# Performance work log

Measured on AMD Instinct MI355X. Metric: run time of the kernel, lower is better.

The kernel has to match this reference:

```python
import jax, jax.numpy as jnp
import numpy as np

S, B, D_DEC, D_ALIGN, D_ENC = 1024, 64, 1024, 1024, 1024


def setup_inputs() -> dict:
    key = jax.random.key(0)
    ks = jax.random.split(key, 6)
    scale = 1.0 / np.sqrt(D_DEC)
    return {
        "s_tm1": jax.random.normal(ks[0], (B, D_DEC), jnp.float32),
        "xs_h": jax.random.normal(ks[1], (S, B, D_ENC), jnp.float32),
        "uh": jax.random.normal(ks[2], (S, B, D_ALIGN), jnp.float32),
        "xs_mask": jnp.ones((S, B), jnp.float32),
        "sa_w": jax.random.normal(ks[3], (D_ALIGN, D_DEC), jnp.float32) * scale,
        "sa_b": jnp.zeros((D_ALIGN,), jnp.float32),
        "a1_w": jax.random.normal(ks[4], (1, D_ALIGN), jnp.float32) * scale,
        "a1_b": jnp.zeros((1,), jnp.float32),
    }


def reference(s_tm1, xs_h, uh, xs_mask, sa_w, sa_b, a1_w, a1_b):
    # sa(s_tm1): [B, align]
    sa_s = s_tm1 @ sa_w.T + sa_b
    # broadcast-add over seq dim, tanh, then a1 (align -> 1), squeeze -> [S, B]
    h = jnp.tanh(sa_s[None, :, :] + uh)                  # [S, B, align]
    e = jnp.einsum('sba,a->sb', h, a1_w[0]) + a1_b[0]    # [S, B]
    # masked softmax over dim 0 (seq)
    ex = jnp.exp(e - jnp.max(e, axis=0, keepdims=True))
    ex = ex * xs_mask
    e_ij = ex / jnp.sum(ex, axis=0, keepdims=True)       # [S, B]
    # weighted sum over seq: [B, D_enc]
    attend = jnp.einsum('sb,sbd->bd', e_ij, xs_h)
    return (e_ij, attend)
```

## Files before the change

### kernel.cpp

```cpp
#include <hip/hip_runtime.h>
#include <hip/hip_bf16.h>

#define S_DIM 1024
#define B_DIM 64
#define A_DIM 1024

#define K2_CONST 2.8853900817779268f

#define K_TILE 64
#define KSPLIT 16
#define A_TILE 64
#define SSPLIT 8
#define S_CHUNK 128
#define NIT (S_CHUNK / 4)

typedef float f4 __attribute__((ext_vector_type(4)));

__device__ __forceinline__ float fast_exp2(float x) { return __builtin_amdgcn_exp2f(x); }
__device__ __forceinline__ float fast_rcp(float x)  { return __builtin_amdgcn_rcpf(x); }

__global__ __launch_bounds__(256) void gemm_partial_kernel(
    const float* __restrict__ s_tm1,
    const float* __restrict__ sa_w,
    float* __restrict__ part)
{
    __shared__ float sW[K_TILE][68];
    __shared__ float sS[K_TILE][68];
    const int a0 = blockIdx.x * A_TILE;
    const int k0 = blockIdx.y * K_TILE;
    const int t  = threadIdx.x;

    #pragma unroll
    for (int i = 0; i < 4; ++i) {
        int idx = t + 256 * i;
        int row = idx >> 4;
        int c4  = (idx & 15) * 4;
        f4 v = __builtin_nontemporal_load((const f4*)(sa_w + (size_t)(a0 + row) * 1024 + k0 + c4));
        sW[c4 + 0][row] = v.x; sW[c4 + 1][row] = v.y;
        sW[c4 + 2][row] = v.z; sW[c4 + 3][row] = v.w;
        f4 u = *(const f4*)(s_tm1 + (size_t)row * 1024 + k0 + c4);
        sS[c4 + 0][row] = u.x; sS[c4 + 1][row] = u.y;
        sS[c4 + 2][row] = u.z; sS[c4 + 3][row] = u.w;
    }
    __syncthreads();

    const int ta = (t & 15) * 4;
    const int tb = (t >> 4) * 4;
    float acc[4][4] = {};
    #pragma unroll 8
    for (int k = 0; k < K_TILE; ++k) {
        f4 wa = *(const f4*)&sW[k][ta];
        f4 sb = *(const f4*)&sS[k][tb];
        float wv[4] = {wa.x, wa.y, wa.z, wa.w};
        float sv[4] = {sb.x, sb.y, sb.z, sb.w};
        #pragma unroll
        for (int i = 0; i < 4; ++i)
            #pragma unroll
            for (int j = 0; j < 4; ++j)
                acc[i][j] = fmaf(wv[i], sv[j], acc[i][j]);
    }

    float* outp = part + (size_t)blockIdx.y * (B_DIM * 1024);
    #pragma unroll
    for (int j = 0; j < 4; ++j) {
        f4 v = {acc[0][j], acc[1][j], acc[2][j], acc[3][j]};
        *(f4*)(outp + (size_t)(tb + j) * 1024 + a0 + ta) = v;
    }
}

__global__ __launch_bounds__(256) void gemm_reduce_kernel(
    const float* __restrict__ part, const float* __restrict__ sa_b,
    float* __restrict__ ksa)
{
    int idx = blockIdx.x * 256 + threadIdx.x;
    int a = idx & 1023;
    float s = sa_b[a];
    #pragma unroll
    for (int kz = 0; kz < KSPLIT; ++kz)
        s += part[(size_t)kz * 65536 + idx];
    ksa[idx] = K2_CONST * s;
}

template <int AUX>
__device__ __forceinline__ void stage_row(const float* g, float* lds_base, int lane) {
    #pragma unroll
    for (int j = 0; j < 4; ++j) {
        __builtin_amdgcn_global_load_lds(
            (const void*)(g + lane * 4 + j * 256),
            (void*)((char*)lds_base + j * 1024),
            16, 0, AUX);
    }
}

__global__ __launch_bounds__(256) void fused_kernel(
    const float* __restrict__ uh,
    const float* __restrict__ xs_h,
    const float* __restrict__ ksa,
    const float* __restrict__ a1_w,
    const float* __restrict__ xs_mask,
    float* __restrict__ ex_buf,
    float* __restrict__ psum,
    float* __restrict__ part)
{
    const int b    = blockIdx.x;
    const int sz   = blockIdx.y;
    const int s0   = sz * S_CHUNK;
    const int t    = threadIdx.x;
    const int lane = t & 63;
    const int w    = t >> 6;

    __shared__ float s_stage[4][4][1024];
    __shared__ float s_ex[S_CHUNK];
    __shared__ float s_mask[S_CHUNK];

    if (t < S_CHUNK) s_mask[t] = xs_mask[(size_t)(s0 + t) * B_DIM + b];

    const f4* sap = (const f4*)(ksa + (size_t)b * 1024);
    const f4* awp = (const f4*)a1_w;
    f4 sv[4], aw[4];
    #pragma unroll
    for (int j = 0; j < 4; ++j) { sv[j] = sap[lane + 64 * j]; aw[j] = awp[lane + 64 * j]; }

    __syncthreads();

    f4 acc4[4];
    #pragma unroll
    for (int j = 0; j < 4; ++j) { acc4[j].x = 0.f; acc4[j].y = 0.f; acc4[j].z = 0.f; acc4[j].w = 0.f; }

    {
        const size_t ro = ((size_t)(s0 + w) * B_DIM + b) * 1024;
        stage_row<2>(uh + ro,   &s_stage[w][0][0], lane);
        stage_row<0>(xs_h + ro, &s_stage[w][2][0], lane);
    }

    #pragma unroll 1
    for (int k = 0; k < NIT; ++k) {
        const int cur = k & 1;
        const int nxt = cur ^ 1;
        const int i   = w + 4 * k;

        const int kn = (k < NIT - 1) ? (k + 1) : (NIT - 1);
        const size_t rn = ((size_t)(s0 + w + 4 * kn) * B_DIM + b) * 1024;
        stage_row<2>(uh + rn,   &s_stage[w][nxt][0], lane);
        stage_row<0>(xs_h + rn, &s_stage[w][2 + nxt][0], lane);

        asm volatile("s_waitcnt vmcnt(8)" ::: "memory");
        __builtin_amdgcn_sched_barrier(0);

        const f4* ub = (const f4*)&s_stage[w][cur][0];
        const f4* xb = (const f4*)&s_stage[w][2 + cur][0];
        f4 u[4], x[4];
        #pragma unroll
        for (int j = 0; j < 4; ++j) { u[j] = ub[lane + 64 * j]; x[j] = xb[lane + 64 * j]; }

        float acc = 0.f;
        #pragma unroll
        for (int j = 0; j < 4; ++j) {
            float t0 = fast_exp2(fmaf(K2_CONST, u[j].x, sv[j].x));
            float t1 = fast_exp2(fmaf(K2_CONST, u[j].y, sv[j].y));
            float t2 = fast_exp2(fmaf(K2_CONST, u[j].z, sv[j].z));
            float t3 = fast_exp2(fmaf(K2_CONST, u[j].w, sv[j].w));
            acc = fmaf(aw[j].x, fast_rcp(1.0f + t0), acc);
            acc = fmaf(aw[j].y, fast_rcp(1.0f + t1), acc);
            acc = fmaf(aw[j].z, fast_rcp(1.0f + t2), acc);
            acc = fmaf(aw[j].w, fast_rcp(1.0f + t3), acc);
        }
        #pragma unroll
        for (int off = 32; off; off >>= 1) acc += __shfl_xor(acc, off);

        float ex = fast_exp2(-K2_CONST * acc) * s_mask[i];
        if (lane == 0) s_ex[i] = ex;

        #pragma unroll
        for (int j = 0; j < 4; ++j) {
            acc4[j].x = fmaf(ex, x[j].x, acc4[j].x);
            acc4[j].y = fmaf(ex, x[j].y, acc4[j].y);
            acc4[j].z = fmaf(ex, x[j].z, acc4[j].z);
            acc4[j].w = fmaf(ex, x[j].w, acc4[j].w);
        }
    }

    asm volatile("s_waitcnt vmcnt(0)" ::: "memory");
    __builtin_amdgcn_sched_barrier(0);

    f4* red = (f4*)&s_stage[w][0][0];
    #pragma unroll
    for (int j = 0; j < 4; ++j) red[lane + 64 * j] = acc4[j];
    __syncthreads();

    f4 r = ((const f4*)&s_stage[0][0][0])[t];
    #pragma unroll
    for (int ww = 1; ww < 4; ++ww) {
        f4 q = ((const f4*)&s_stage[ww][0][0])[t];
        r.x += q.x; r.y += q.y; r.z += q.z; r.w += q.w;
    }
    ((f4*)part)[((size_t)sz * B_DIM + b) * 256 + t] = r;

    if (t < S_CHUNK)
        ex_buf[(size_t)(s0 + t) * B_DIM + b] = s_ex[t];

    if (w == 0) {
        float v = s_ex[lane] + s_ex[lane + 64];
        #pragma unroll
        for (int off = 32; off; off >>= 1) v += __shfl_xor(v, off);
        if (lane == 0) psum[sz * B_DIM + b] = v;
    }
}

__global__ __launch_bounds__(256) void finalize_kernel(
    const float* __restrict__ ex_buf, const float* __restrict__ part,
    const float* __restrict__ psum,
    float* __restrict__ eij_out, float* __restrict__ att_out)
{
    const int blk = blockIdx.x;
    const int t = threadIdx.x;
    if (blk < 256) {
        int idx = blk * 256 + t;
        int b = idx & 63;
        float ssum = 0.f;
        #pragma unroll
        for (int sz = 0; sz < SSPLIT; ++sz) ssum += psum[sz * B_DIM + b];
        eij_out[idx] = ex_buf[idx] * (1.0f / ssum);
    } else {
        int idx = (blk - 256) * 256 + t;
        int b = idx >> 10;
        float ssum = 0.f;
        #pragma unroll
        for (int sz = 0; sz < SSPLIT; ++sz) ssum += psum[sz * B_DIM + b];
        float acc = 0.f;
        #pragma unroll
        for (int sz = 0; sz < SSPLIT; ++sz) acc += part[(size_t)sz * 65536 + idx];
        att_out[idx] = acc * (1.0f / ssum);
    }
}

extern "C" void kernel_launch(void* const* d_in, const int* in_sizes, int n_in,
                              void* d_out, int out_size, void* d_ws, size_t ws_size,
                              hipStream_t stream) {
    const float* s_tm1   = (const float*)d_in[0];
    const float* xs_h    = (const float*)d_in[1];
    const float* uh      = (const float*)d_in[2];
    const float* xs_mask = (const float*)d_in[3];
    const float* sa_w    = (const float*)d_in[4];
    const float* sa_b    = (const float*)d_in[5];
    const float* a1_w    = (const float*)d_in[6];

    float* eij_out = (float*)d_out;
    float* att_out = (float*)d_out + S_DIM * B_DIM;

    float* part_gemm = (float*)d_ws;
    float* ksa       = part_gemm + (size_t)KSPLIT * B_DIM * 1024;
    float* ex_buf    = ksa + 65536;
    float* part_att  = ex_buf + 65536;
    float* psum      = part_att + (size_t)SSPLIT * B_DIM * 1024;

    gemm_partial_kernel<<<dim3(A_DIM / A_TILE, KSPLIT), 256, 0, stream>>>(s_tm1, sa_w, part_gemm);
    gemm_reduce_kernel<<<65536 / 256, 256, 0, stream>>>(part_gemm, sa_b, ksa);
    fused_kernel<<<dim3(B_DIM, SSPLIT), 256, 0, stream>>>(uh, xs_h, ksa, a1_w, xs_mask,
                                                          ex_buf, psum, part_att);
    finalize_kernel<<<512, 256, 0, stream>>>(ex_buf, part_att, psum, eij_out, att_out);
}
```

Measured before the change: 101.3 us.

## Prefetch uh two rows ahead and issue xs_h loads just in time

Reworks the LDS staging pipeline in the fused attention kernel. The uh rows now use a triple buffer prefetched two iterations ahead, and each xs_h row goes into a single buffer loaded at the start of its own iteration. Separate vmcnt waits let the tanh/score work start before the xs_h data has arrived, giving uh loads more latency hiding. The trade-off is that the xs_h load is no longer prefetched, so the weighted-sum step may stall on it. LDS use stays at 64KB, and an extra barrier is added before the reduction reuses the buffer.

```diff
diff --git a/kernel.cpp b/kernel.cpp
--- a/kernel.cpp
+++ b/kernel.cpp
@@ -82,12 +82,12 @@
 }
 
 template <int AUX>
-__device__ __forceinline__ void stage_row(const float* g, float* lds_base, int lane) {
+__device__ __forceinline__ void stage4(const float* g, float* lds, int lane) {
     #pragma unroll
     for (int j = 0; j < 4; ++j) {
         __builtin_amdgcn_global_load_lds(
             (const void*)(g + lane * 4 + j * 256),
-            (void*)((char*)lds_base + j * 1024),
+            (void*)((char*)lds + j * 1024),
             16, 0, AUX);
     }
 }
@@ -109,7 +109,8 @@
     const int lane = t & 63;
     const int w    = t >> 6;
 
-    __shared__ float s_stage[4][4][1024];
+    __shared__ float s_uh[3][4][1024];
+    __shared__ float s_xs[4][1024];
     __shared__ float s_ex[S_CHUNK];
     __shared__ float s_mask[S_CHUNK];
 
@@ -127,31 +128,26 @@
     #pragma unroll
     for (int j = 0; j < 4; ++j) { acc4[j].x = 0.f; acc4[j].y = 0.f; acc4[j].z = 0.f; acc4[j].w = 0.f; }
 
-    {
-        const size_t ro = ((size_t)(s0 + w) * B_DIM + b) * 1024;
-        stage_row<2>(uh + ro,   &s_stage[w][0][0], lane);
-        stage_row<0>(xs_h + ro, &s_stage[w][2][0], lane);
-    }
+    #define ROFF(kk) ((((size_t)(s0 + w + 4 * (kk))) * B_DIM + b) * 1024)
+
+    stage4<2>(uh + ROFF(0), &s_uh[0][w][0], lane);
+    stage4<2>(uh + ROFF(1), &s_uh[1][w][0], lane);
 
     #pragma unroll 1
     for (int k = 0; k < NIT; ++k) {
-        const int cur = k & 1;
-        const int nxt = cur ^ 1;
-        const int i   = w + 4 * k;
-
-        const int kn = (k < NIT - 1) ? (k + 1) : (NIT - 1);
-        const size_t rn = ((size_t)(s0 + w + 4 * kn) * B_DIM + b) * 1024;
-        stage_row<2>(uh + rn,   &s_stage[w][nxt][0], lane);
-        stage_row<0>(xs_h + rn, &s_stage[w][2 + nxt][0], lane);
-
-        asm volatile("s_waitcnt vmcnt(8)" ::: "memory");
+        const int i = w + 4 * k;
+
+        stage4<0>(xs_h + ROFF(k), &s_xs[w][0], lane);
+        const int kn = (k + 2 < NIT) ? (k + 2) : (NIT - 1);
+        stage4<2>(uh + ROFF(kn), &s_uh[(k + 2) % 3][w][0], lane);
+
+        asm volatile("s_waitcnt vmcnt(12)" ::: "memory");
         __builtin_amdgcn_sched_barrier(0);
 
-        const f4* ub = (const f4*)&s_stage[w][cur][0];
-        const f4* xb = (const f4*)&s_stage[w][2 + cur][0];
-        f4 u[4], x[4];
-        #pragma unroll
-        for (int j = 0; j < 4; ++j) { u[j] = ub[lane + 64 * j]; x[j] = xb[lane + 64 * j]; }
+        const f4* ub = (const f4*)&s_uh[k % 3][w][0];
+        f4 u[4];
+        #pragma unroll
+        for (int j = 0; j < 4; ++j) u[j] = ub[lane + 64 * j];
 
         float acc = 0.f;
         #pragma unroll
@@ -171,27 +167,34 @@
         float ex = fast_exp2(-K2_CONST * acc) * s_mask[i];
         if (lane == 0) s_ex[i] = ex;
 
+        asm volatile("s_waitcnt vmcnt(4)" ::: "memory");
+        __builtin_amdgcn_sched_barrier(0);
+
+        const f4* xb = (const f4*)&s_xs[w][0];
         #pragma unroll
         for (int j = 0; j < 4; ++j) {
-            acc4[j].x = fmaf(ex, x[j].x, acc4[j].x);
-            acc4[j].y = fmaf(ex, x[j].y, acc4[j].y);
-            acc4[j].z = fmaf(ex, x[j].z, acc4[j].z);
-            acc4[j].w = fmaf(ex, x[j].w, acc4[j].w);
+            f4 x = xb[lane + 64 * j];
+            acc4[j].x = fmaf(ex, x.x, acc4[j].x);
+            acc4[j].y = fmaf(ex, x.y, acc4[j].y);
+            acc4[j].z = fmaf(ex, x.z, acc4[j].z);
+            acc4[j].w = fmaf(ex, x.w, acc4[j].w);
         }
     }
+    #undef ROFF
 
     asm volatile("s_waitcnt vmcnt(0)" ::: "memory");
     __builtin_amdgcn_sched_barrier(0);
-
-    f4* red = (f4*)&s_stage[w][0][0];
-    #pragma unroll
-    for (int j = 0; j < 4; ++j) red[lane + 64 * j] = acc4[j];
-    __syncthreads();
-
-    f4 r = ((const f4*)&s_stage[0][0][0])[t];
+    __syncthreads();
+
+    f4* red = (f4*)&s_uh[0][0][0];
+    #pragma unroll
+    for (int j = 0; j < 4; ++j) red[(w << 8) + lane + 64 * j] = acc4[j];
+    __syncthreads();
+
+    f4 r = red[t];
     #pragma unroll
     for (int ww = 1; ww < 4; ++ww) {
-        f4 q = ((const f4*)&s_stage[ww][0][0])[t];
+        f4 q = red[(ww << 8) + t];
         r.x += q.x; r.y += q.y; r.z += q.z; r.w += q.w;
     }
     ((f4*)part)[((size_t)sz * B_DIM + b) * 256 + t] = r;
```

New measurement: 113.8 us. 1.12x slower.
